# Performance work log

Measured on AMD Instinct MI355X. Metric: run time of the kernel, lower is better.

## Reference

```python
import jax, jax.numpy as jnp
import numpy as np

B, S, D = 4, 2048, 768
H = 12
DH = D // H
FF = 4 * D
EPS = 1e-5


def _layernorm(x, g, b):
    mu = jnp.mean(x, axis=-1, keepdims=True)
    var = jnp.mean(jnp.square(x - mu), axis=-1, keepdims=True)
    return (x - mu) * jax.lax.rsqrt(var + EPS) * g + b


def setup_inputs() -> dict:
    key = jax.random.key(0)
    ks = jax.random.split(key, 16)
    s_d = 1.0 / np.sqrt(D)
    s_ff = 1.0 / np.sqrt(FF)
    inp = {
        "x": jax.random.normal(ks[0], (B, S, D), jnp.float32),
        # LayerNorm 1
        "ln1_g": jnp.ones((D,), jnp.float32),
        "ln1_b": jnp.zeros((D,), jnp.float32),
        # attention linears (stored as [in, out], i.e. already transposed)
        "Wq": jax.random.normal(ks[1], (D, D), jnp.float32) * s_d,
        "bq": jax.random.normal(ks[2], (D,), jnp.float32) * s_d,
        "Wk": jax.random.normal(ks[3], (D, D), jnp.float32) * s_d,
        "bk": jax.random.normal(ks[4], (D,), jnp.float32) * s_d,
        "Wv": jax.random.normal(ks[5], (D, D), jnp.float32) * s_d,
        "bv": jax.random.normal(ks[6], (D,), jnp.float32) * s_d,
        "Wo": jax.random.normal(ks[7], (D, D), jnp.float32) * s_d,
        "bo": jax.random.normal(ks[8], (D,), jnp.float32) * s_d,
        # LayerNorm 2
        "ln2_g": jnp.ones((D,), jnp.float32),
        "ln2_b": jnp.zeros((D,), jnp.float32),
        # feed-forward (bias always on, per torch code)
        "W1": jax.random.normal(ks[9], (D, FF), jnp.float32) * s_d,
        "b1": jax.random.normal(ks[10], (FF,), jnp.float32) * s_d,
        "W2": jax.random.normal(ks[11], (FF, D), jnp.float32) * s_ff,
        "b2": jax.random.normal(ks[12], (D,), jnp.float32) * s_ff,
    }
    return inp


def reference(x, ln1_g, ln1_b, Wq, bq, Wk, bk, Wv, bv, Wo, bo,
              ln2_g, ln2_b, W1, b1, W2, b2):
    # --- attention branch (pre-LN) ---
    h = _layernorm(x, ln1_g, ln1_b)
    q = (h @ Wq + bq).reshape(B, S, H, DH).transpose(0, 2, 1, 3)  # [B,H,S,DH]
    k = (h @ Wk + bk).reshape(B, S, H, DH).transpose(0, 2, 1, 3)
    v = (h @ Wv + bv).reshape(B, S, H, DH).transpose(0, 2, 1, 3)
    scores = jnp.einsum("bhqd,bhkd->bhqk", q, k) / np.sqrt(DH)
    causal = jnp.tril(jnp.ones((S, S), bool))
    scores = jnp.where(causal, scores, -jnp.inf)
    attn = jax.nn.softmax(scores, axis=-1)
    out = jnp.einsum("bhqk,bhkd->bhqd", attn, v)
    out = out.transpose(0, 2, 1, 3).reshape(B, S, D)
    x = x + (out @ Wo + bo)
    # --- feed-forward branch (pre-LN, exact GELU) ---
    h2 = _layernorm(x, ln2_g, ln2_b)
    ff = jax.nn.gelu(h2 @ W1 + b1, approximate=False) @ W2 + b2
    return x + ff
```

## Files before the change

kernel.cpp:

```cpp
#include <hip/hip_runtime.h>
#include <math.h>

#define B_ 4
#define S_ 2048
#define D_ 768
#define H_ 12
#define DH_ 64
#define FF_ 3072
#define LDQ (3*D_)

using short8  = __attribute__((ext_vector_type(8))) short;
using f32x4   = __attribute__((ext_vector_type(4))) float;
using f32x16  = __attribute__((ext_vector_type(16))) float;
using float4v = __attribute__((ext_vector_type(4))) float;
using ushort4v= __attribute__((ext_vector_type(4))) unsigned short;

__device__ __forceinline__ unsigned short f2bf(float f) {
  unsigned u = __builtin_bit_cast(unsigned, f);
  u += 0x7FFFu + ((u >> 16) & 1u);
  return (unsigned short)(u >> 16);
}

__device__ __forceinline__ unsigned cvt_pk_bf16(float a, float b) {
  unsigned r;
  asm("v_cvt_pk_bf16_f32 %0, %1, %2" : "=v"(r) : "v"(a), "v"(b));
  return r;
}

__device__ __forceinline__ float gelu_tanh(float x) {
  float x2 = x * x;
  float y  = x * fmaf(0.0356774081f, x2, 0.7978845608f);
  float e  = exp2f(y * 2.885390082f);
  float t  = 1.0f - 2.0f / (e + 1.0f);
  float hx = 0.5f * x;
  return fmaf(hx, t, hx);
}

__device__ __forceinline__ void gload16(const void* g, void* l) {
  __builtin_amdgcn_global_load_lds(
      (const __attribute__((address_space(1))) unsigned*)g,
      (__attribute__((address_space(3))) unsigned*)l, 16, 0, 0);
}

__global__ __launch_bounds__(256) void transpose_cast_multi_kernel(
    const float* __restrict__ Wq, const float* __restrict__ Wk,
    const float* __restrict__ Wv, const float* __restrict__ Wo,
    const float* __restrict__ W1, const float* __restrict__ W2,
    unsigned short* __restrict__ WqT, unsigned short* __restrict__ WkT,
    unsigned short* __restrict__ WvT, unsigned short* __restrict__ WoT,
    unsigned short* __restrict__ W1T, unsigned short* __restrict__ W2T) {
  __shared__ float tile[32][33];
  int bid = blockIdx.x;
  const float* in; unsigned short* out; int K, N, t;
  if (bid < 2304) {
    int seg = bid / 576; t = bid % 576; K = D_; N = D_;
    in  = seg == 0 ? Wq  : seg == 1 ? Wk  : seg == 2 ? Wv  : Wo;
    out = seg == 0 ? WqT : seg == 1 ? WkT : seg == 2 ? WvT : WoT;
  } else if (bid < 4608) {
    t = bid - 2304; K = D_; N = FF_; in = W1; out = W1T;
  } else {
    t = bid - 4608; K = FF_; N = D_; in = W2; out = W2T;
  }
  int ntk = K / 32;
  int k0 = (t % ntk) * 32, n0 = (t / ntk) * 32;
  int tx = threadIdx.x, ty = threadIdx.y;
#pragma unroll
  for (int i = 0; i < 4; i++)
    tile[ty + 8*i][tx] = in[(size_t)(k0 + ty + 8*i) * N + n0 + tx];
  __syncthreads();
#pragma unroll
  for (int i = 0; i < 4; i++)
    out[(size_t)(n0 + ty + 8*i) * K + k0 + tx] = f2bf(tile[tx][ty + 8*i]);
}

__global__ void bias_cat_kernel(const float* __restrict__ bq, const float* __restrict__ bk,
                                const float* __restrict__ bv, float* __restrict__ dst) {
  int i = blockIdx.x * 256 + threadIdx.x;
  if (i >= 3 * D_) return;
  float v;
  if (i < D_)            v = bq[i];
  else if (i < 2 * D_)   v = bk[i - D_];
  else                   v = bv[i - 2 * D_];
  dst[i] = v;
}

__global__ __launch_bounds__(256) void layernorm_kernel(
    const float* __restrict__ x, const float* __restrict__ g,
    const float* __restrict__ b, unsigned short* __restrict__ out) {
  int wave = threadIdx.x >> 6, lane = threadIdx.x & 63;
  int row = blockIdx.x * 4 + wave;
  const float* xr = x + (size_t)row * D_;
  float4v v[3];
  float sum = 0.f, sq = 0.f;
#pragma unroll
  for (int i = 0; i < 3; i++) {
    v[i] = reinterpret_cast<const float4v*>(xr)[lane + 64*i];
#pragma unroll
    for (int j = 0; j < 4; j++) { sum += v[i][j]; sq += v[i][j]*v[i][j]; }
  }
#pragma unroll
  for (int d = 1; d < 64; d <<= 1) { sum += __shfl_xor(sum, d); sq += __shfl_xor(sq, d); }
  float mu   = sum * (1.0f / D_);
  float var  = sq  * (1.0f / D_) - mu * mu;
  float rstd = rsqrtf(var + 1e-5f);
  unsigned short* orow = out + (size_t)row * D_;
#pragma unroll
  for (int i = 0; i < 3; i++) {
    int idx = (lane + 64*i) * 4;
    ushort4v o;
#pragma unroll
    for (int j = 0; j < 4; j++)
      o[j] = f2bf((v[i][j] - mu) * rstd * g[idx + j] + b[idx + j]);
    *reinterpret_cast<ushort4v*>(orow + idx) = o;
  }
}

#define EPI_QKV   0
#define EPI_OPROJ 1
#define EPI_GELU  2
#define EPI_FINAL 3

template<int EPI>
__global__ __launch_bounds__(256) void gemm_kernel(
    const unsigned short* __restrict__ A, int lda,
    const unsigned short* __restrict__ BT, int K,
    const float* __restrict__ bias,
    const float* __restrict__ resid,
    float* __restrict__ outf,
    unsigned short* __restrict__ outh,
    int ldo, float ascale, int nN) {
  __shared__ __attribute__((aligned(16))) unsigned short Ls[3][128*64];
  int tid = threadIdx.x;
  int wave = tid >> 6, lane = tid & 63;
  int lrow = lane & 15, lk = lane >> 4;
  int bid = blockIdx.x;
  int xcd = bid & 7, j = bid >> 3;
  int nM8 = gridDim.x / (8 * nN);
  int m0 = (xcd * nM8 + j / nN) * 128;
  int n0 = (j % nN) * 128;
  int wm = (wave >> 1) * 64, wn = (wave & 1) * 64;

  auto STAGE = [&](int buf, int k0) {
#pragma unroll
    for (int i = 0; i < 4; i++) {
      int ch = i * 256 + tid;
      int row = ch >> 3, s8 = ch & 7;
      int m = s8 ^ (row & 7);
      const unsigned short* src = (m < 4)
        ? A  + (size_t)(m0 + row) * lda + k0 + m * 8
        : BT + (size_t)(n0 + row) * K   + k0 + (m - 4) * 8;
      gload16(src, &Ls[buf][(i*256 + wave*64) * 8]);
    }
  };

  f32x4 acc[4][4] = {};
  int nt = K / 32;
  STAGE(0, 0);
  STAGE(1, 32);
  for (int t = 0; t < nt; t++) {
    if (t + 1 < nt) { asm volatile("s_waitcnt vmcnt(4)" ::: "memory"); }
    else            { asm volatile("s_waitcnt vmcnt(0)" ::: "memory"); }
    __builtin_amdgcn_s_barrier();
    const unsigned short* Lc = Ls[t % 3];
    short8 af[4], bf[4];
#pragma unroll
    for (int mi = 0; mi < 4; mi++) {
      int row = wm + mi*16 + lrow;
      af[mi] = *reinterpret_cast<const short8*>(&Lc[row*64 + ((lk ^ (row & 7)) * 8)]);
    }
#pragma unroll
    for (int ni = 0; ni < 4; ni++) {
      int row = wn + ni*16 + lrow;
      bf[ni] = *reinterpret_cast<const short8*>(&Lc[row*64 + (((4 + lk) ^ (row & 7)) * 8)]);
    }
    if (t + 2 < nt) STAGE((t + 2) % 3, (t + 2) * 32);
    __builtin_amdgcn_s_setprio(1);
#pragma unroll
    for (int mi = 0; mi < 4; mi++)
#pragma unroll
      for (int ni = 0; ni < 4; ni++)
        acc[mi][ni] = __builtin_amdgcn_mfma_f32_16x16x32_bf16(af[mi], bf[ni], acc[mi][ni], 0, 0, 0);
    __builtin_amdgcn_s_setprio(0);
  }
#pragma unroll
  for (int mi = 0; mi < 4; mi++) {
#pragma unroll
    for (int ni = 0; ni < 4; ni++) {
#pragma unroll
      for (int r = 0; r < 4; r++) {
        int gm = m0 + wm + mi*16 + (lane >> 4)*4 + r;
        int gn = n0 + wn + ni*16 + lrow;
        float v = acc[mi][ni][r] + bias[gn];
        if constexpr (EPI == EPI_QKV) {
          if (gn < D_) v *= ascale;
          float nb = __shfl_xor(v, 1);
          if (!(lane & 1))
            *reinterpret_cast<unsigned*>(&outh[(size_t)gm * ldo + gn]) = cvt_pk_bf16(v, nb);
        } else if constexpr (EPI == EPI_OPROJ) {
          size_t idx = (size_t)gm * ldo + gn;
          outf[idx] = v + resid[idx];
        } else if constexpr (EPI == EPI_GELU) {
          float gv = gelu_tanh(v);
          float nb = __shfl_xor(gv, 1);
          if (!(lane & 1))
            *reinterpret_cast<unsigned*>(&outh[(size_t)gm * ldo + gn]) = cvt_pk_bf16(gv, nb);
        } else {
          size_t idx = (size_t)gm * ldo + gn;
          outf[idx] = v + resid[idx];
        }
      }
    }
  }
}

__global__ __launch_bounds__(256, 3) void attn_kernel(
    const unsigned short* __restrict__ qkv,
    unsigned short* __restrict__ o) {
  __shared__ __attribute__((aligned(16))) unsigned short Ks[2][64*64];
  __shared__ __attribute__((aligned(16))) unsigned short VT[2][64*64];
  int tid = threadIdx.x;
  int wave = tid >> 6, lane = tid & 63;
  int ql = lane & 31, hi = lane >> 5;
  int bid = blockIdx.x;
  int xcd = bid & 7, r = bid >> 3;
  int bh = xcd * 6 + (r % 6);
  int qtile = 15 - (r / 6);
  int bb = bh / H_, hh = bh % H_;
  const unsigned short* qb = qkv + (size_t)bb * S_ * LDQ + hh * DH_;
  const unsigned short* kb = qb + D_;
  const unsigned short* vb = qb + 2 * D_;

  int sr = tid >> 2;
  int sc16 = (tid & 3) * 16;
  int kp = tid & 31, dh0 = (tid >> 5) * 8;
  uint4 krA, krB, vrA, vrB;

  auto LOADR = [&](int kb0) {
    const unsigned short* ksrc = kb + (size_t)(kb0 + sr) * LDQ + sc16;
    krA = *reinterpret_cast<const uint4*>(ksrc);
    krB = *reinterpret_cast<const uint4*>(ksrc + 8);
    const unsigned short* vsrc = vb + (size_t)(kb0 + 2*kp) * LDQ + dh0;
    vrA = *reinterpret_cast<const uint4*>(vsrc);
    vrB = *reinterpret_cast<const uint4*>(vsrc + LDQ);
  };
  auto WRITE = [&](int buf) {
    int sw = (sr & 7) << 4;
    int cb = sc16 * 2;
    *reinterpret_cast<uint4*>(&Ks[buf][(sr*128 + (cb ^ sw)) >> 1]) = krA;
    *reinterpret_cast<uint4*>(&Ks[buf][(sr*128 + ((cb + 16) ^ sw)) >> 1]) = krB;
    union { uint4 u4; unsigned short s[8]; } a, b;
    a.u4 = vrA; b.u4 = vrB;
#pragma unroll
    for (int j2 = 0; j2 < 8; j2++) {
      int row = dh0 + j2, sw2 = (row & 7) << 4;
      *reinterpret_cast<unsigned*>(&VT[buf][(row*128 + ((4*kp) ^ sw2)) >> 1]) =
          (unsigned)a.s[j2] | ((unsigned)b.s[j2] << 16);
    }
  };

  int q0 = qtile * 128;
  int qw = q0 + wave * 32;
  int myq = qw + ql;

  short8 qf[4];
#pragma unroll
  for (int dblk = 0; dblk < 4; dblk++)
    qf[dblk] = *reinterpret_cast<const short8*>(qb + (size_t)myq * LDQ + dblk*16 + hi*8);

  f32x16 oaccT[2] = {};
  float mst = -1e30f, lst = 0.f;
  int nt = q0 / 64 + 2;

  auto TILE = [&](int kt, int cur) {
    int kb0 = kt * 64;
    bool has_next = (kt + 1 < nt);
    if (has_next) LOADR((kt + 1) * 64);

    if (kb0 <= qw + 31) {
      f32x16 sc[2] = {};
      __builtin_amdgcn_s_setprio(1);
#pragma unroll
      for (int dblk = 0; dblk < 4; dblk++) {
#pragma unroll
        for (int blk = 0; blk < 2; blk++) {
          int row = blk*32 + ql;
          int sw = (row & 7) << 4;
          short8 kf = *reinterpret_cast<const short8*>(
              &Ks[cur][(row*128 + (((unsigned)(dblk*32 + hi*16)) ^ sw)) >> 1]);
          sc[blk] = __builtin_amdgcn_mfma_f32_32x32x16_bf16(kf, qf[dblk], sc[blk], 0, 0, 0);
        }
      }
      __builtin_amdgcn_s_setprio(0);
      bool full = (kb0 + 63 <= qw);
      if (!full) {
#pragma unroll
        for (int blk = 0; blk < 2; blk++)
#pragma unroll
          for (int r2 = 0; r2 < 16; r2++) {
            int key = kb0 + blk*32 + (r2 & 3) + 8*(r2 >> 2) + 4*hi;
            if (key > myq) sc[blk][r2] = -1e30f;
          }
      }
      float pm0 = -1e30f, pm1 = -1e30f, pm2 = -1e30f, pm3 = -1e30f;
#pragma unroll
      for (int blk = 0; blk < 2; blk++)
#pragma unroll
        for (int g = 0; g < 4; g++) {
          pm0 = fmaxf(pm0, sc[blk][4*g]);
          pm1 = fmaxf(pm1, sc[blk][4*g+1]);
          pm2 = fmaxf(pm2, sc[blk][4*g+2]);
          pm3 = fmaxf(pm3, sc[blk][4*g+3]);
        }
      float mx = fmaxf(fmaxf(pm0, pm1), fmaxf(pm2, pm3));
      mx = fmaxf(mx, __shfl_xor(mx, 32));
      if (!__all(mx <= mst + 8.0f)) {
        float mnew = fmaxf(mst, mx);
        float fac = exp2f(mst - mnew);
        lst *= fac;
#pragma unroll
        for (int db = 0; db < 2; db++)
#pragma unroll
          for (int r2 = 0; r2 < 16; r2++) oaccT[db][r2] *= fac;
        mst = mnew;
      }
      short8 pa[4];
      float rs = 0.f;
#pragma unroll
      for (int b = 0; b < 2; b++) {
#pragma unroll
        for (int so = 0; so < 2; so++) {
          float p0 = exp2f(sc[b][8*so + 0] - mst);
          float p1 = exp2f(sc[b][8*so + 1] - mst);
          float p2 = exp2f(sc[b][8*so + 2] - mst);
          float p3 = exp2f(sc[b][8*so + 3] - mst);
          float p4 = exp2f(sc[b][8*so + 4] - mst);
          float p5 = exp2f(sc[b][8*so + 5] - mst);
          float p6 = exp2f(sc[b][8*so + 6] - mst);
          float p7 = exp2f(sc[b][8*so + 7] - mst);
          rs += ((p0 + p1) + (p2 + p3)) + ((p4 + p5) + (p6 + p7));
          unsigned W0 = cvt_pk_bf16(p0, p1);
          unsigned W1 = cvt_pk_bf16(p2, p3);
          unsigned W2 = cvt_pk_bf16(p4, p5);
          unsigned W3 = cvt_pk_bf16(p6, p7);
          asm volatile("v_permlane32_swap_b32 %0, %1" : "+v"(W0), "+v"(W2));
          asm volatile("v_permlane32_swap_b32 %0, %1" : "+v"(W1), "+v"(W3));
          union { uint4 u; short8 s; } cvtu;
          cvtu.u.x = W0; cvtu.u.y = W1; cvtu.u.z = W2; cvtu.u.w = W3;
          pa[2*b + so] = cvtu.s;
        }
      }
      rs += __shfl_xor(rs, 32);
      lst += rs;
      __builtin_amdgcn_s_setprio(1);
#pragma unroll
      for (int ks = 0; ks < 4; ks++) {
        int cb = ks*32 + hi*16;
#pragma unroll
        for (int db = 0; db < 2; db++) {
          int row = db*32 + ql;
          int sw = (row & 7) << 4;
          short8 vf = *reinterpret_cast<const short8*>(&VT[cur][(row*128 + (cb ^ sw)) >> 1]);
          oaccT[db] = __builtin_amdgcn_mfma_f32_32x32x16_bf16(vf, pa[ks], oaccT[db], 0, 0, 0);
        }
      }
      __builtin_amdgcn_s_setprio(0);
    }

    if (has_next) WRITE(cur ^ 1);
    __syncthreads();
  };

  LOADR(0);
  WRITE(0);
  __syncthreads();
  for (int kt = 0; kt < nt; kt += 2) {
    TILE(kt, 0);
    TILE(kt + 1, 1);
  }

  float inv = 1.0f / lst;
  unsigned short* ob = o + ((size_t)(bb * S_ + myq)) * D_ + hh * DH_;
#pragma unroll
  for (int db = 0; db < 2; db++)
#pragma unroll
    for (int g = 0; g < 8; g++) {
      int r2 = 2 * g;
      int dh = db*32 + (r2 & 3) + 8*(r2 >> 2) + 4*hi;
      unsigned pk = cvt_pk_bf16(oaccT[db][r2] * inv, oaccT[db][r2+1] * inv);
      *reinterpret_cast<unsigned*>(ob + dh) = pk;
    }
}

extern "C" void kernel_launch(void* const* d_in, const int* in_sizes, int n_in,
                              void* d_out, int out_size, void* d_ws, size_t ws_size,
                              hipStream_t stream) {
  (void)in_sizes; (void)n_in; (void)out_size; (void)ws_size;
  const float* x    = (const float*)d_in[0];
  const float* ln1g = (const float*)d_in[1];
  const float* ln1b = (const float*)d_in[2];
  const float* Wq   = (const float*)d_in[3];
  const float* bq   = (const float*)d_in[4];
  const float* Wk   = (const float*)d_in[5];
  const float* bk   = (const float*)d_in[6];
  const float* Wv   = (const float*)d_in[7];
  const float* bv   = (const float*)d_in[8];
  const float* Wo   = (const float*)d_in[9];
  const float* bo   = (const float*)d_in[10];
  const float* ln2g = (const float*)d_in[11];
  const float* ln2b = (const float*)d_in[12];
  const float* W1   = (const float*)d_in[13];
  const float* b1   = (const float*)d_in[14];
  const float* W2   = (const float*)d_in[15];
  const float* b2   = (const float*)d_in[16];
  float* out = (float*)d_out;

  char* ws = (char*)d_ws;
  size_t off = 0;
  auto alloc = [&](size_t bytes) {
    char* p = ws + off;
    off += (bytes + 255) & ~(size_t)255;
    return p;
  };
  unsigned short* WqT = (unsigned short*)alloc((size_t)D_*D_*2);
  unsigned short* WkT = (unsigned short*)alloc((size_t)D_*D_*2);
  unsigned short* WvT = (unsigned short*)alloc((size_t)D_*D_*2);
  unsigned short* WoT = (unsigned short*)alloc((size_t)D_*D_*2);
  unsigned short* W1T = (unsigned short*)alloc((size_t)D_*FF_*2);
  unsigned short* W2T = (unsigned short*)alloc((size_t)FF_*D_*2);
  unsigned short* h   = (unsigned short*)alloc((size_t)B_*S_*D_*2);
  unsigned short* qkv = (unsigned short*)alloc((size_t)B_*S_*LDQ*2);
  unsigned short* ob  = (unsigned short*)alloc((size_t)B_*S_*D_*2);
  float* bias_cat     = (float*)alloc((size_t)3*D_*4);
  unsigned short* ffb = qkv;
  unsigned short* h2  = h;

  const float qscale = 0.125f * 1.4426950408889634f;

  dim3 tb(32, 8);
  transpose_cast_multi_kernel<<<6912, tb, 0, stream>>>(
      Wq, Wk, Wv, Wo, W1, W2, WqT, WkT, WvT, WoT, W1T, W2T);
  bias_cat_kernel<<<9, 256, 0, stream>>>(bq, bk, bv, bias_cat);

  layernorm_kernel<<<(B_*S_)/4, 256, 0, stream>>>(x, ln1g, ln1b, h);

  gemm_kernel<EPI_QKV><<<dim3(64*18), 256, 0, stream>>>(
      h, D_, WqT, D_, bias_cat, nullptr, nullptr, qkv, LDQ, qscale, 18);

  attn_kernel<<<dim3(768), 256, 0, stream>>>(qkv, ob);

  gemm_kernel<EPI_OPROJ><<<dim3(64*6), 256, 0, stream>>>(
      ob, D_, WoT, D_, bo, x, out, nullptr, D_, 1.0f, 6);

  layernorm_kernel<<<(B_*S_)/4, 256, 0, stream>>>(out, ln2g, ln2b, h2);

  gemm_kernel<EPI_GELU><<<dim3(64*24), 256, 0, stream>>>(
      h2, D_, W1T, D_, b1, nullptr, nullptr, ffb, FF_, 1.0f, 24);

  gemm_kernel<EPI_FINAL><<<dim3(64*6), 256, 0, stream>>>(
      ffb, FF_, W2T, FF_, b2, out, out, nullptr, D_, 1.0f, 6);
}
```

Before: 264.4 us.

## Switch GEMM to double-buffered LDS with occupancy hint and hoisted addressing

Moves the GEMM K-loop from a 3-stage LDS ring (two tiles in flight) to a 2-buffer scheme. The next tile is issued at the top of each iteration, and the loop waits for all loads plus a barrier after the MFMAs. Global source and LDS fragment offsets are now computed once outside the loop, and launch_bounds asks for 5 blocks per CU. This cuts LDS per block to raise occupancy and trims address arithmetic, at the cost of shallower prefetch and a full vmcnt(0) stall every iteration.

```diff
diff --git a/kernel.cpp b/kernel.cpp
--- a/kernel.cpp
+++ b/kernel.cpp
@@ -121,7 +121,7 @@
 #define EPI_FINAL 3
 
 template<int EPI>
-__global__ __launch_bounds__(256) void gemm_kernel(
+__global__ __launch_bounds__(256, 5) void gemm_kernel(
     const unsigned short* __restrict__ A, int lda,
     const unsigned short* __restrict__ BT, int K,
     const float* __restrict__ bias,
@@ -129,7 +129,7 @@
     float* __restrict__ outf,
     unsigned short* __restrict__ outh,
     int ldo, float ascale, int nN) {
-  __shared__ __attribute__((aligned(16))) unsigned short Ls[3][128*64];
+  __shared__ __attribute__((aligned(16))) unsigned short Ls[2][128*64];
   int tid = threadIdx.x;
   int wave = tid >> 6, lane = tid & 63;
   int lrow = lane & 15, lk = lane >> 4;
@@ -140,40 +140,52 @@
   int n0 = (j % nN) * 128;
   int wm = (wave >> 1) * 64, wn = (wave & 1) * 64;
 
+  const unsigned short* srcBase[4];
+  int ldsDst[4];
+#pragma unroll
+  for (int i = 0; i < 4; i++) {
+    int ch = i * 256 + tid;
+    int row = ch >> 3, s8 = ch & 7;
+    int m = s8 ^ (row & 7);
+    srcBase[i] = (m < 4)
+      ? A  + (size_t)(m0 + row) * lda + m * 8
+      : BT + (size_t)(n0 + row) * K   + (m - 4) * 8;
+    ldsDst[i] = (i*256 + wave*64) * 8;
+  }
   auto STAGE = [&](int buf, int k0) {
 #pragma unroll
-    for (int i = 0; i < 4; i++) {
-      int ch = i * 256 + tid;
-      int row = ch >> 3, s8 = ch & 7;
-      int m = s8 ^ (row & 7);
-      const unsigned short* src = (m < 4)
-        ? A  + (size_t)(m0 + row) * lda + k0 + m * 8
-        : BT + (size_t)(n0 + row) * K   + k0 + (m - 4) * 8;
-      gload16(src, &Ls[buf][(i*256 + wave*64) * 8]);
-    }
+    for (int i = 0; i < 4; i++)
+      gload16(srcBase[i] + k0, &Ls[buf][ldsDst[i]]);
   };
+
+  int offA[4], offB[4];
+#pragma unroll
+  for (int mi = 0; mi < 4; mi++) {
+    int row = wm + mi*16 + lrow;
+    offA[mi] = row*64 + ((lk ^ (row & 7)) * 8);
+  }
+#pragma unroll
+  for (int ni = 0; ni < 4; ni++) {
+    int row = wn + ni*16 + lrow;
+    offB[ni] = row*64 + (((4 + lk) ^ (row & 7)) * 8);
+  }
 
   f32x4 acc[4][4] = {};
   int nt = K / 32;
   STAGE(0, 0);
-  STAGE(1, 32);
+  asm volatile("s_waitcnt vmcnt(0)" ::: "memory");
+  __builtin_amdgcn_s_barrier();
   for (int t = 0; t < nt; t++) {
-    if (t + 1 < nt) { asm volatile("s_waitcnt vmcnt(4)" ::: "memory"); }
-    else            { asm volatile("s_waitcnt vmcnt(0)" ::: "memory"); }
-    __builtin_amdgcn_s_barrier();
-    const unsigned short* Lc = Ls[t % 3];
+    int cur = t & 1;
+    if (t + 1 < nt) STAGE(cur ^ 1, (t + 1) * 32);
+    const unsigned short* Lc = Ls[cur];
     short8 af[4], bf[4];
 #pragma unroll
-    for (int mi = 0; mi < 4; mi++) {
-      int row = wm + mi*16 + lrow;
-      af[mi] = *reinterpret_cast<const short8*>(&Lc[row*64 + ((lk ^ (row & 7)) * 8)]);
-    }
-#pragma unroll
-    for (int ni = 0; ni < 4; ni++) {
-      int row = wn + ni*16 + lrow;
-      bf[ni] = *reinterpret_cast<const short8*>(&Lc[row*64 + (((4 + lk) ^ (row & 7)) * 8)]);
-    }
-    if (t + 2 < nt) STAGE((t + 2) % 3, (t + 2) * 32);
+    for (int mi = 0; mi < 4; mi++)
+      af[mi] = *reinterpret_cast<const short8*>(&Lc[offA[mi]]);
+#pragma unroll
+    for (int ni = 0; ni < 4; ni++)
+      bf[ni] = *reinterpret_cast<const short8*>(&Lc[offB[ni]]);
     __builtin_amdgcn_s_setprio(1);
 #pragma unroll
     for (int mi = 0; mi < 4; mi++)
@@ -181,6 +193,8 @@
       for (int ni = 0; ni < 4; ni++)
         acc[mi][ni] = __builtin_amdgcn_mfma_f32_16x16x32_bf16(af[mi], bf[ni], acc[mi][ni], 0, 0, 0);
     __builtin_amdgcn_s_setprio(0);
+    asm volatile("s_waitcnt vmcnt(0)" ::: "memory");
+    __builtin_amdgcn_s_barrier();
   }
 #pragma unroll
   for (int mi = 0; mi < 4; mi++) {
```

Result: slower. 577.8 us (+118.5%).
